# Kernel optimization log

Hardware: AMD Instinct MI355X
Metric: run time of the kernel (lower is better)

The kernel has to match this reference:

```python
import jax, jax.numpy as jnp
import numpy as np

INPUT_SIZE = 34
HIDDEN = 4
NUM_CLASSES = 3
B, T = 4096, 200


def setup_inputs() -> dict:
    key = jax.random.key(0)
    ks = jax.random.split(key, 8)
    k = 1.0 / np.sqrt(HIDDEN)  # torch default uniform init bound
    u = lambda kk, shape: jax.random.uniform(kk, shape, jnp.float32, -k, k)
    x = jax.random.normal(ks[0], (B, T, INPUT_SIZE), jnp.float32)
    W_ih = u(ks[1], (4 * HIDDEN, INPUT_SIZE))   # gate order: i, f, g, o
    W_hh = u(ks[2], (4 * HIDDEN, HIDDEN))
    b_ih = u(ks[3], (4 * HIDDEN,))
    b_hh = u(ks[4], (4 * HIDDEN,))
    W_fc = u(ks[5], (NUM_CLASSES, HIDDEN))
    b_fc = u(ks[6], (NUM_CLASSES,))
    return {"x": x, "W_ih": W_ih, "W_hh": W_hh, "b_ih": b_ih,
            "b_hh": b_hh, "W_fc": W_fc, "b_fc": b_fc}


def reference(x, W_ih, W_hh, b_ih, b_hh, W_fc, b_fc):
    Bsz = x.shape[0]
    H = W_hh.shape[1]
    # Precompute input contributions for all timesteps: [B, T, 4H]
    x_gates = jnp.einsum('btd,gd->btg', x, W_ih) + b_ih + b_hh
    x_gates = jnp.swapaxes(x_gates, 0, 1)  # [T, B, 4H] for scan

    def step(carry, xg_t):
        h, c = carry
        gates = xg_t + h @ W_hh.T          # [B, 4H]
        i, f, g, o = jnp.split(gates, 4, axis=-1)
        i = jax.nn.sigmoid(i)
        f = jax.nn.sigmoid(f)
        g = jnp.tanh(g)
        o = jax.nn.sigmoid(o)
        c = f * c + i * g
        h = o * jnp.tanh(c)
        return (h, c), None

    h0 = jnp.zeros((Bsz, H), x.dtype)
    c0 = jnp.zeros((Bsz, H), x.dtype)
    (h_last, _), _ = jax.lax.scan(step, (h0, c0), x_gates)
    # dropout is identity in eval mode
    return h_last @ W_fc.T + b_fc  # [B, num_classes]
```

## Files before the change

### kernel.cpp

```cpp
#include <hip/hip_runtime.h>

#define B_SZ 4096
#define T_SZ 200
#define IN_SZ 34

__device__ __forceinline__ float sigf(float x) {
    return 1.0f / (1.0f + __expf(-x));
}
__device__ __forceinline__ float tanh_f(float x) {
    return 2.0f / (1.0f + __expf(-2.0f * x)) - 1.0f;
}

__device__ __forceinline__ float quad_bcast0(float v) {
    int s = __float_as_int(v);
    return __int_as_float(__builtin_amdgcn_update_dpp(s, s, 0x00, 0xf, 0xf, true));
}
__device__ __forceinline__ float quad_bcast1(float v) {
    int s = __float_as_int(v);
    return __int_as_float(__builtin_amdgcn_update_dpp(s, s, 0x55, 0xf, 0xf, true));
}
__device__ __forceinline__ float quad_bcast2(float v) {
    int s = __float_as_int(v);
    return __int_as_float(__builtin_amdgcn_update_dpp(s, s, 0xAA, 0xf, 0xf, true));
}
__device__ __forceinline__ float quad_bcast3(float v) {
    int s = __float_as_int(v);
    return __int_as_float(__builtin_amdgcn_update_dpp(s, s, 0xFF, 0xf, 0xf, true));
}

__global__ __launch_bounds__(256) void xgates_kernel(
    const float* __restrict__ x, const float* __restrict__ W_ih,
    const float* __restrict__ b_ih, const float* __restrict__ b_hh,
    float* __restrict__ xg) {
  __shared__ float xs[256 * IN_SZ];
  const float4* src = reinterpret_cast<const float4*>(x + (size_t)blockIdx.x * 256 * IN_SZ);
  float4* dst = reinterpret_cast<float4*>(xs);
  for (int i = threadIdx.x; i < 256 * IN_SZ / 4; i += 256) dst[i] = src[i];
  __syncthreads();

  float xr[IN_SZ];
  const float2* rp = reinterpret_cast<const float2*>(&xs[threadIdx.x * IN_SZ]);
  #pragma unroll
  for (int k = 0; k < IN_SZ / 2; ++k) {
    float2 v = rp[k];
    xr[2 * k] = v.x;
    xr[2 * k + 1] = v.y;
  }
  float acc[16];
  #pragma unroll
  for (int g = 0; g < 16; ++g) acc[g] = b_ih[g] + b_hh[g];
  #pragma unroll
  for (int k = 0; k < IN_SZ; ++k) {
    #pragma unroll
    for (int g = 0; g < 16; ++g)
      acc[g] = fmaf(xr[k], W_ih[g * IN_SZ + k], acc[g]);
  }
  size_t row = (size_t)blockIdx.x * 256 + threadIdx.x;
  float4* op = reinterpret_cast<float4*>(xg + row * 16);
  #pragma unroll
  for (int j = 0; j < 4; ++j)
    op[j] = make_float4(acc[j], acc[4 + j], acc[8 + j], acc[12 + j]);
}

#define U_SZ 10
__global__ __launch_bounds__(64) void lstm_scan(
    const float* __restrict__ xg, const float* __restrict__ W_hh,
    const float* __restrict__ W_fc, const float* __restrict__ b_fc,
    float* __restrict__ out) {
  int tid = blockIdx.x * 64 + threadIdx.x;
  int b = tid >> 2;
  int j = tid & 3;
  float Wi[4], Wf[4], Wg[4], Wo[4];
  #pragma unroll
  for (int k = 0; k < 4; ++k) {
    Wi[k] = W_hh[(0 + j) * 4 + k];
    Wf[k] = W_hh[(4 + j) * 4 + k];
    Wg[k] = W_hh[(8 + j) * 4 + k];
    Wo[k] = W_hh[(12 + j) * 4 + k];
  }
  float h[4] = {0.f, 0.f, 0.f, 0.f};
  float c = 0.f;

  auto step = [&](float4 g4) {
    float pi = g4.x, pf = g4.y, pg = g4.z, po = g4.w;
    #pragma unroll
    for (int k = 0; k < 4; ++k) {
      pi = fmaf(Wi[k], h[k], pi);
      pf = fmaf(Wf[k], h[k], pf);
      pg = fmaf(Wg[k], h[k], pg);
      po = fmaf(Wo[k], h[k], po);
    }
    float iv = sigf(pi);
    float fv = sigf(pf);
    float gv = tanh_f(pg);
    float ov = sigf(po);
    c = fmaf(fv, c, iv * gv);
    float hj = ov * tanh_f(c);
    h[0] = quad_bcast0(hj);
    h[1] = quad_bcast1(hj);
    h[2] = quad_bcast2(hj);
    h[3] = quad_bcast3(hj);
  };

  const float4* xp = reinterpret_cast<const float4*>(xg) + (size_t)b * (T_SZ * 4) + j;
  float4 bufA[U_SZ], bufB[U_SZ];
  #pragma unroll
  for (int u = 0; u < U_SZ; ++u) bufA[u] = xp[4 * u];

  #pragma unroll 1
  for (int blk = 0; blk < 20; blk += 2) {
    const float4* p1 = xp + (size_t)(blk + 1) * (4 * U_SZ);
    #pragma unroll
    for (int u = 0; u < U_SZ; ++u) bufB[u] = p1[4 * u];
    #pragma unroll
    for (int u = 0; u < U_SZ; ++u) step(bufA[u]);
    if (blk + 2 < 20) {
      const float4* p2 = xp + (size_t)(blk + 2) * (4 * U_SZ);
      #pragma unroll
      for (int u = 0; u < U_SZ; ++u) bufA[u] = p2[4 * u];
    }
    #pragma unroll
    for (int u = 0; u < U_SZ; ++u) step(bufB[u]);
  }

  if (j < 3) {
    float acc = b_fc[j];
    #pragma unroll
    for (int k = 0; k < 4; ++k) acc = fmaf(W_fc[j * 4 + k], h[k], acc);
    out[b * 3 + j] = acc;
  }
}

__global__ __launch_bounds__(256) void lstm_fused(
    const float* __restrict__ x, const float* __restrict__ W_ih,
    const float* __restrict__ W_hh, const float* __restrict__ b_ih,
    const float* __restrict__ b_hh, const float* __restrict__ W_fc,
    const float* __restrict__ b_fc, float* __restrict__ out) {
  __shared__ float Ws[16 * IN_SZ];
  for (int i = threadIdx.x; i < 16 * IN_SZ; i += 256) Ws[i] = W_ih[i];
  __syncthreads();
  int tid = blockIdx.x * 256 + threadIdx.x;
  int b = tid >> 2;
  int j = tid & 3;
  float bi = b_ih[0 + j] + b_hh[0 + j];
  float bf = b_ih[4 + j] + b_hh[4 + j];
  float bg = b_ih[8 + j] + b_hh[8 + j];
  float bo = b_ih[12 + j] + b_hh[12 + j];
  float Wi[4], Wf[4], Wg[4], Wo[4];
  #pragma unroll
  for (int k = 0; k < 4; ++k) {
    Wi[k] = W_hh[(0 + j) * 4 + k];
    Wf[k] = W_hh[(4 + j) * 4 + k];
    Wg[k] = W_hh[(8 + j) * 4 + k];
    Wo[k] = W_hh[(12 + j) * 4 + k];
  }
  float h[4] = {0.f, 0.f, 0.f, 0.f};
  float c = 0.f;
  const float2* xp = reinterpret_cast<const float2*>(x + (size_t)b * T_SZ * IN_SZ);
  int lbase = (threadIdx.x & 63) & ~3;
  for (int t = 0; t < T_SZ; ++t) {
    float xr[IN_SZ];
    #pragma unroll
    for (int k = 0; k < IN_SZ / 2; ++k) {
      float2 v = xp[(size_t)t * (IN_SZ / 2) + k];
      xr[2 * k] = v.x;
      xr[2 * k + 1] = v.y;
    }
    float pi = bi, pf = bf, pg = bg, po = bo;
    #pragma unroll
    for (int k = 0; k < IN_SZ; ++k) {
      pi = fmaf(xr[k], Ws[(0 + j) * IN_SZ + k], pi);
      pf = fmaf(xr[k], Ws[(4 + j) * IN_SZ + k], pf);
      pg = fmaf(xr[k], Ws[(8 + j) * IN_SZ + k], pg);
      po = fmaf(xr[k], Ws[(12 + j) * IN_SZ + k], po);
    }
    #pragma unroll
    for (int k = 0; k < 4; ++k) {
      pi = fmaf(Wi[k], h[k], pi);
      pf = fmaf(Wf[k], h[k], pf);
      pg = fmaf(Wg[k], h[k], pg);
      po = fmaf(Wo[k], h[k], po);
    }
    float iv = sigf(pi);
    float fv = sigf(pf);
    float gv = tanh_f(pg);
    float ov = sigf(po);
    c = fmaf(fv, c, iv * gv);
    float hj = ov * tanh_f(c);
    h[0] = __shfl(hj, lbase + 0);
    h[1] = __shfl(hj, lbase + 1);
    h[2] = __shfl(hj, lbase + 2);
    h[3] = __shfl(hj, lbase + 3);
  }
  if (j < 3) {
    float acc = b_fc[j];
    #pragma unroll
    for (int k = 0; k < 4; ++k) acc = fmaf(W_fc[j * 4 + k], h[k], acc);
    out[b * 3 + j] = acc;
  }
}

extern "C" void kernel_launch(void* const* d_in, const int* in_sizes, int n_in,
                              void* d_out, int out_size, void* d_ws, size_t ws_size,
                              hipStream_t stream) {
  const float* x    = (const float*)d_in[0];
  const float* W_ih = (const float*)d_in[1];
  const float* W_hh = (const float*)d_in[2];
  const float* b_ih = (const float*)d_in[3];
  const float* b_hh = (const float*)d_in[4];
  const float* W_fc = (const float*)d_in[5];
  const float* b_fc = (const float*)d_in[6];
  float* out = (float*)d_out;

  const size_t need = (size_t)B_SZ * T_SZ * 16 * sizeof(float);
  if (ws_size >= need) {
    float* xg = (float*)d_ws;
    hipLaunchKernelGGL(xgates_kernel, dim3(B_SZ * T_SZ / 256), dim3(256), 0, stream,
                       x, W_ih, b_ih, b_hh, xg);
    hipLaunchKernelGGL(lstm_scan, dim3(B_SZ * 4 / 64), dim3(64), 0, stream,
                       xg, W_hh, W_fc, b_fc, out);
  } else {
    hipLaunchKernelGGL(lstm_fused, dim3(B_SZ * 4 / 256), dim3(256), 0, stream,
                       x, W_ih, W_hh, b_ih, b_hh, W_fc, b_fc, out);
  }
}
```

Before: 98.97 us.

## Fuse input projection and LSTM scan into one kernel with fp16 LDS gate staging

Replaces the two-kernel path (input projection to global workspace, then scan) with a single kernel per 8 sequences. The whole workgroup first computes input gate projections, split over quads with DPP reductions, and stores them as packed fp16 in LDS. Then 8 lanes per wave run the recurrence reading from LDS. This removes the global round trip of the gate tensor, at the cost of fp16 rounding of the pre-activations and a serial scan phase that uses only a few lanes per wave.

```diff
diff --git a/kernel.cpp b/kernel.cpp
--- a/kernel.cpp
+++ b/kernel.cpp
@@ -1,8 +1,13 @@
 #include <hip/hip_runtime.h>
+#include <hip/hip_fp16.h>
 
 #define B_SZ 4096
 #define T_SZ 200
 #define IN_SZ 34
+#define GSEQ 8
+#define NWG (B_SZ / GSEQ)
+#define ROWS (GSEQ * T_SZ)
+#define LDS_T_STRIDE 33
 
 __device__ __forceinline__ float sigf(float x) {
     return 1.0f / (1.0f + __expf(-x));
@@ -27,176 +32,137 @@
     int s = __float_as_int(v);
     return __int_as_float(__builtin_amdgcn_update_dpp(s, s, 0xFF, 0xf, 0xf, true));
 }
-
-__global__ __launch_bounds__(256) void xgates_kernel(
-    const float* __restrict__ x, const float* __restrict__ W_ih,
-    const float* __restrict__ b_ih, const float* __restrict__ b_hh,
-    float* __restrict__ xg) {
-  __shared__ float xs[256 * IN_SZ];
-  const float4* src = reinterpret_cast<const float4*>(x + (size_t)blockIdx.x * 256 * IN_SZ);
-  float4* dst = reinterpret_cast<float4*>(xs);
-  for (int i = threadIdx.x; i < 256 * IN_SZ / 4; i += 256) dst[i] = src[i];
-  __syncthreads();
-
-  float xr[IN_SZ];
-  const float2* rp = reinterpret_cast<const float2*>(&xs[threadIdx.x * IN_SZ]);
-  #pragma unroll
-  for (int k = 0; k < IN_SZ / 2; ++k) {
-    float2 v = rp[k];
-    xr[2 * k] = v.x;
-    xr[2 * k + 1] = v.y;
-  }
-  float acc[16];
-  #pragma unroll
-  for (int g = 0; g < 16; ++g) acc[g] = b_ih[g] + b_hh[g];
-  #pragma unroll
-  for (int k = 0; k < IN_SZ; ++k) {
-    #pragma unroll
-    for (int g = 0; g < 16; ++g)
-      acc[g] = fmaf(xr[k], W_ih[g * IN_SZ + k], acc[g]);
-  }
-  size_t row = (size_t)blockIdx.x * 256 + threadIdx.x;
-  float4* op = reinterpret_cast<float4*>(xg + row * 16);
-  #pragma unroll
-  for (int j = 0; j < 4; ++j)
-    op[j] = make_float4(acc[j], acc[4 + j], acc[8 + j], acc[12 + j]);
+__device__ __forceinline__ float quad_red(float v) {
+    int s = __float_as_int(v);
+    v += __int_as_float(__builtin_amdgcn_update_dpp(s, s, 0xB1, 0xf, 0xf, true));
+    s = __float_as_int(v);
+    v += __int_as_float(__builtin_amdgcn_update_dpp(s, s, 0x4E, 0xf, 0xf, true));
+    return v;
+}
+__device__ __forceinline__ float qsel(float a0, float a1, float a2, float a3, int q) {
+    return q == 0 ? a0 : q == 1 ? a1 : q == 2 ? a2 : a3;
 }
 
-#define U_SZ 10
-__global__ __launch_bounds__(64) void lstm_scan(
-    const float* __restrict__ xg, const float* __restrict__ W_hh,
-    const float* __restrict__ W_fc, const float* __restrict__ b_fc,
-    float* __restrict__ out) {
-  int tid = blockIdx.x * 64 + threadIdx.x;
-  int b = tid >> 2;
-  int j = tid & 3;
-  float Wi[4], Wf[4], Wg[4], Wo[4];
-  #pragma unroll
-  for (int k = 0; k < 4; ++k) {
-    Wi[k] = W_hh[(0 + j) * 4 + k];
-    Wf[k] = W_hh[(4 + j) * 4 + k];
-    Wg[k] = W_hh[(8 + j) * 4 + k];
-    Wo[k] = W_hh[(12 + j) * 4 + k];
-  }
-  float h[4] = {0.f, 0.f, 0.f, 0.f};
-  float c = 0.f;
-
-  auto step = [&](float4 g4) {
-    float pi = g4.x, pf = g4.y, pg = g4.z, po = g4.w;
-    #pragma unroll
-    for (int k = 0; k < 4; ++k) {
-      pi = fmaf(Wi[k], h[k], pi);
-      pf = fmaf(Wf[k], h[k], pf);
-      pg = fmaf(Wg[k], h[k], pg);
-      po = fmaf(Wo[k], h[k], po);
-    }
-    float iv = sigf(pi);
-    float fv = sigf(pf);
-    float gv = tanh_f(pg);
-    float ov = sigf(po);
-    c = fmaf(fv, c, iv * gv);
-    float hj = ov * tanh_f(c);
-    h[0] = quad_bcast0(hj);
-    h[1] = quad_bcast1(hj);
-    h[2] = quad_bcast2(hj);
-    h[3] = quad_bcast3(hj);
-  };
-
-  const float4* xp = reinterpret_cast<const float4*>(xg) + (size_t)b * (T_SZ * 4) + j;
-  float4 bufA[U_SZ], bufB[U_SZ];
-  #pragma unroll
-  for (int u = 0; u < U_SZ; ++u) bufA[u] = xp[4 * u];
-
-  #pragma unroll 1
-  for (int blk = 0; blk < 20; blk += 2) {
-    const float4* p1 = xp + (size_t)(blk + 1) * (4 * U_SZ);
-    #pragma unroll
-    for (int u = 0; u < U_SZ; ++u) bufB[u] = p1[4 * u];
-    #pragma unroll
-    for (int u = 0; u < U_SZ; ++u) step(bufA[u]);
-    if (blk + 2 < 20) {
-      const float4* p2 = xp + (size_t)(blk + 2) * (4 * U_SZ);
-      #pragma unroll
-      for (int u = 0; u < U_SZ; ++u) bufA[u] = p2[4 * u];
-    }
-    #pragma unroll
-    for (int u = 0; u < U_SZ; ++u) step(bufB[u]);
-  }
-
-  if (j < 3) {
-    float acc = b_fc[j];
-    #pragma unroll
-    for (int k = 0; k < 4; ++k) acc = fmaf(W_fc[j * 4 + k], h[k], acc);
-    out[b * 3 + j] = acc;
-  }
-}
-
-__global__ __launch_bounds__(256) void lstm_fused(
+__global__ __launch_bounds__(256, 2) void lstm_all(
     const float* __restrict__ x, const float* __restrict__ W_ih,
     const float* __restrict__ W_hh, const float* __restrict__ b_ih,
     const float* __restrict__ b_hh, const float* __restrict__ W_fc,
     const float* __restrict__ b_fc, float* __restrict__ out) {
-  __shared__ float Ws[16 * IN_SZ];
-  for (int i = threadIdx.x; i < 16 * IN_SZ; i += 256) Ws[i] = W_ih[i];
-  __syncthreads();
-  int tid = blockIdx.x * 256 + threadIdx.x;
-  int b = tid >> 2;
-  int j = tid & 3;
-  float bi = b_ih[0 + j] + b_hh[0 + j];
-  float bf = b_ih[4 + j] + b_hh[4 + j];
-  float bg = b_ih[8 + j] + b_hh[8 + j];
-  float bo = b_ih[12 + j] + b_hh[12 + j];
-  float Wi[4], Wf[4], Wg[4], Wo[4];
+  __shared__ uint2 gl[T_SZ * LDS_T_STRIDE];
+  const int tid = threadIdx.x;
+  const int q = tid & 3;
+  const int rowslot = tid >> 2;
+  const int wg = blockIdx.x;
+
+  float wk[9][16];
   #pragma unroll
-  for (int k = 0; k < 4; ++k) {
-    Wi[k] = W_hh[(0 + j) * 4 + k];
-    Wf[k] = W_hh[(4 + j) * 4 + k];
-    Wg[k] = W_hh[(8 + j) * 4 + k];
-    Wo[k] = W_hh[(12 + j) * 4 + k];
+  for (int m = 0; m < 8; ++m) {
+    int k = 2 * q + ((m >> 1) << 3) + (m & 1);
+    #pragma unroll
+    for (int g = 0; g < 16; ++g) wk[m][g] = W_ih[g * IN_SZ + k];
   }
-  float h[4] = {0.f, 0.f, 0.f, 0.f};
-  float c = 0.f;
-  const float2* xp = reinterpret_cast<const float2*>(x + (size_t)b * T_SZ * IN_SZ);
-  int lbase = (threadIdx.x & 63) & ~3;
-  for (int t = 0; t < T_SZ; ++t) {
-    float xr[IN_SZ];
+  #pragma unroll
+  for (int g = 0; g < 16; ++g)
+    wk[8][g] = (q < 2) ? W_ih[g * IN_SZ + 32 + q] : 0.f;
+  float bias4[4];
+  #pragma unroll
+  for (int z = 0; z < 4; ++z) bias4[z] = b_ih[z * 4 + q] + b_hh[z * 4 + q];
+
+  const float* xbase = x + (size_t)wg * (ROWS * IN_SZ);
+  #pragma unroll 1
+  for (int i = 0; i < ROWS / 64; ++i) {
+    int ri = rowslot + 64 * i;
+    const char* rp = reinterpret_cast<const char*>(xbase + (size_t)ri * IN_SZ);
+    float xv[9];
     #pragma unroll
-    for (int k = 0; k < IN_SZ / 2; ++k) {
-      float2 v = xp[(size_t)t * (IN_SZ / 2) + k];
-      xr[2 * k] = v.x;
-      xr[2 * k + 1] = v.y;
+    for (int m2 = 0; m2 < 4; ++m2) {
+      float2 v = *reinterpret_cast<const float2*>(rp + q * 8 + m2 * 32);
+      xv[2 * m2] = v.x;
+      xv[2 * m2 + 1] = v.y;
     }
-    float pi = bi, pf = bf, pg = bg, po = bo;
+    xv[8] = (q < 2) ? *reinterpret_cast<const float*>(rp + 128 + q * 4) : 0.f;
+
+    float acc[16];
     #pragma unroll
-    for (int k = 0; k < IN_SZ; ++k) {
-      pi = fmaf(xr[k], Ws[(0 + j) * IN_SZ + k], pi);
-      pf = fmaf(xr[k], Ws[(4 + j) * IN_SZ + k], pf);
-      pg = fmaf(xr[k], Ws[(8 + j) * IN_SZ + k], pg);
-      po = fmaf(xr[k], Ws[(12 + j) * IN_SZ + k], po);
+    for (int g = 0; g < 16; ++g) acc[g] = 0.f;
+    #pragma unroll
+    for (int m = 0; m < 9; ++m) {
+      #pragma unroll
+      for (int g = 0; g < 16; ++g) acc[g] = fmaf(xv[m], wk[m][g], acc[g]);
     }
     #pragma unroll
+    for (int g = 0; g < 16; ++g) acc[g] = quad_red(acc[g]);
+    float vi = qsel(acc[0], acc[1], acc[2], acc[3], q) + bias4[0];
+    float vf = qsel(acc[4], acc[5], acc[6], acc[7], q) + bias4[1];
+    float vg = qsel(acc[8], acc[9], acc[10], acc[11], q) + bias4[2];
+    float vo = qsel(acc[12], acc[13], acc[14], acc[15], q) + bias4[3];
+    unsigned s = (unsigned)ri / 200u;
+    unsigned t = (unsigned)ri - s * 200u;
+    union { __half2 h[2]; uint2 v; } u;
+    u.h[0] = __floats2half2_rn(vi, vf);
+    u.h[1] = __floats2half2_rn(vg, vo);
+    gl[t * LDS_T_STRIDE + s * 4 + q] = u.v;
+  }
+  __syncthreads();
+
+  const int l = tid & 63;
+  const int w = tid >> 6;
+  if (l < 8) {
+    const int s = 2 * w + (l >> 2);
+    const int jq = l & 3;
+    float Wi[4], Wf[4], Wg[4], Wo[4];
+    #pragma unroll
     for (int k = 0; k < 4; ++k) {
-      pi = fmaf(Wi[k], h[k], pi);
-      pf = fmaf(Wf[k], h[k], pf);
-      pg = fmaf(Wg[k], h[k], pg);
-      po = fmaf(Wo[k], h[k], po);
+      Wi[k] = W_hh[(0 + jq) * 4 + k];
+      Wf[k] = W_hh[(4 + jq) * 4 + k];
+      Wg[k] = W_hh[(8 + jq) * 4 + k];
+      Wo[k] = W_hh[(12 + jq) * 4 + k];
     }
-    float iv = sigf(pi);
-    float fv = sigf(pf);
-    float gv = tanh_f(pg);
-    float ov = sigf(po);
-    c = fmaf(fv, c, iv * gv);
-    float hj = ov * tanh_f(c);
-    h[0] = __shfl(hj, lbase + 0);
-    h[1] = __shfl(hj, lbase + 1);
-    h[2] = __shfl(hj, lbase + 2);
-    h[3] = __shfl(hj, lbase + 3);
-  }
-  if (j < 3) {
-    float acc = b_fc[j];
-    #pragma unroll
-    for (int k = 0; k < 4; ++k) acc = fmaf(W_fc[j * 4 + k], h[k], acc);
-    out[b * 3 + j] = acc;
+    float h[4] = {0.f, 0.f, 0.f, 0.f};
+    float c = 0.f;
+
+    auto step = [&](uint2 wv) {
+      union { uint2 u; __half2 h2[2]; } v;
+      v.u = wv;
+      float2 p01 = __half22float2(v.h2[0]);
+      float2 p23 = __half22float2(v.h2[1]);
+      float pi = p01.x, pf = p01.y, pg = p23.x, po = p23.y;
+      #pragma unroll
+      for (int k = 0; k < 4; ++k) {
+        pi = fmaf(Wi[k], h[k], pi);
+        pf = fmaf(Wf[k], h[k], pf);
+        pg = fmaf(Wg[k], h[k], pg);
+        po = fmaf(Wo[k], h[k], po);
+      }
+      float iv = sigf(pi);
+      float fv = sigf(pf);
+      float gv = tanh_f(pg);
+      float ov = sigf(po);
+      c = fmaf(fv, c, iv * gv);
+      float hj = ov * tanh_f(c);
+      h[0] = quad_bcast0(hj);
+      h[1] = quad_bcast1(hj);
+      h[2] = quad_bcast2(hj);
+      h[3] = quad_bcast3(hj);
+    };
+
+    const uint2* lp = &gl[s * 4 + jq];
+    #pragma unroll 1
+    for (int tb = 0; tb < 20; ++tb) {
+      uint2 v[10];
+      #pragma unroll
+      for (int u = 0; u < 10; ++u)
+        v[u] = lp[(size_t)(tb * 10 + u) * LDS_T_STRIDE];
+      #pragma unroll
+      for (int u = 0; u < 10; ++u) step(v[u]);
+    }
+
+    if (jq < 3) {
+      float a = b_fc[jq];
+      #pragma unroll
+      for (int k = 0; k < 4; ++k) a = fmaf(W_fc[jq * 4 + k], h[k], a);
+      out[(wg * GSEQ + s) * 3 + jq] = a;
+    }
   }
 }
 
@@ -211,16 +177,8 @@
   const float* W_fc = (const float*)d_in[5];
   const float* b_fc = (const float*)d_in[6];
   float* out = (float*)d_out;
+  (void)in_sizes; (void)n_in; (void)out_size; (void)d_ws; (void)ws_size;
 
-  const size_t need = (size_t)B_SZ * T_SZ * 16 * sizeof(float);
-  if (ws_size >= need) {
-    float* xg = (float*)d_ws;
-    hipLaunchKernelGGL(xgates_kernel, dim3(B_SZ * T_SZ / 256), dim3(256), 0, stream,
-                       x, W_ih, b_ih, b_hh, xg);
-    hipLaunchKernelGGL(lstm_scan, dim3(B_SZ * 4 / 64), dim3(64), 0, stream,
-                       xg, W_hh, W_fc, b_fc, out);
-  } else {
-    hipLaunchKernelGGL(lstm_fused, dim3(B_SZ * 4 / 256), dim3(256), 0, stream,
-                       x, W_ih, W_hh, b_ih, b_hh, W_fc, b_fc, out);
-  }
+  hipLaunchKernelGGL(lstm_all, dim3(NWG), dim3(256), 0, stream,
+                     x, W_ih, W_hh, b_ih, b_hh, W_fc, b_fc, out);
 }
```

New measurement: 188.1 us. 90.0% more time.
